# Kernel tuning notes

Hardware: AMD Instinct MI355X
Metric: run time of the kernel (lower is better)

The kernel has to match this reference:

```python
import jax, jax.numpy as jnp
import numpy as np

VOCAB, D, T, B, H, NCLS = 50000, 128, 512, 512, 100, 4


def setup_inputs() -> dict:
    key = jax.random.key(0)
    ks = jax.random.split(key, 7)
    tokens = jax.random.randint(ks[0], (B, T), 0, VOCAB, dtype=jnp.int32)
    emb = jax.random.normal(ks[1], (VOCAB, D), dtype=jnp.float32) * 0.05
    # Keras LSTM gate order: i, f, c(g), o packed along last dim (4H)
    kernel = jax.random.normal(ks[2], (D, 4 * H), dtype=jnp.float32) * (1.0 / np.sqrt(D))
    rec_kernel = jax.random.normal(ks[3], (H, 4 * H), dtype=jnp.float32) * (1.0 / np.sqrt(H))
    # unit_forget_bias: forget-gate bias initialized to 1
    bias = jnp.zeros((4 * H,), dtype=jnp.float32).at[H:2 * H].set(1.0)
    dense_w = jax.random.normal(ks[4], (H, NCLS), dtype=jnp.float32) * (1.0 / np.sqrt(H))
    dense_b = jnp.zeros((NCLS,), dtype=jnp.float32)
    return {"tokens": tokens, "emb": emb, "kernel": kernel,
            "rec_kernel": rec_kernel, "bias": bias,
            "dense_w": dense_w, "dense_b": dense_b}


def _lstm_last_hidden(x_tbd, kernel, rec_kernel, bias):
    # x_tbd: [T, B, D]. Precompute input projections for all steps (one big GEMM).
    xz = jnp.einsum('tbd,dg->tbg', x_tbd, kernel) + bias  # [T, B, 4H]

    def step(carry, xz_t):
        h, c = carry
        z = xz_t + h @ rec_kernel  # [B, 4H]
        i = jax.nn.sigmoid(z[:, 0 * H:1 * H])
        f = jax.nn.sigmoid(z[:, 1 * H:2 * H])
        g = jnp.tanh(z[:, 2 * H:3 * H])
        o = jax.nn.sigmoid(z[:, 3 * H:4 * H])
        c_new = f * c + i * g
        h_new = o * jnp.tanh(c_new)
        return (h_new, c_new), None

    bsz = x_tbd.shape[1]
    init = (jnp.zeros((bsz, H), x_tbd.dtype), jnp.zeros((bsz, H), x_tbd.dtype))
    (h_last, _), _ = jax.lax.scan(step, init, xz)
    return h_last  # [B, H]


def reference(tokens, emb, kernel, rec_kernel, bias, dense_w, dense_b):
    # Embedding lookup: [B, T] -> [B, T, D]
    x = emb[tokens]
    # SpatialDropout1D and LSTM dropout/recurrent_dropout are identity at inference.
    x_tbd = jnp.transpose(x, (1, 0, 2))  # [T, B, D]
    h = _lstm_last_hidden(x_tbd, kernel, rec_kernel, bias)  # [B, H]
    logits = h @ dense_w + dense_b  # [B, 4]
    return jax.nn.softmax(logits, axis=-1)
```

## Files before the change

kernel.cpp:

```cpp
#include <hip/hip_runtime.h>
#include <hip/hip_bf16.h>

#define VOCAB 50000
#define DD 128
#define TT 512
#define BB 512
#define HH 100
#define NCLS 4
#define NT 25
#define ROWS 4
#define NBLK (BB/ROWS)
#define NTHREADS 512
#define ZS 400

typedef short s16x8 __attribute__((ext_vector_type(8)));
typedef float f32x4 __attribute__((ext_vector_type(4)));

static __device__ __forceinline__ unsigned short f2b(float x) {
    __hip_bfloat16 h = __float2bfloat16(x);
    return __builtin_bit_cast(unsigned short, h);
}
static __device__ __forceinline__ float sigm(float x)  { return __fdividef(1.0f, 1.0f + __expf(-x)); }
static __device__ __forceinline__ float tanhx(float x) { return 1.0f - __fdividef(2.0f, 1.0f + __expf(2.0f * x)); }

#define BARRIER() asm volatile("s_waitcnt lgkmcnt(0)\n\ts_barrier" ::: "memory")

__global__ void cast_emb_k(const float* __restrict__ emb, unsigned short* __restrict__ out, int n4) {
    int i = blockIdx.x * blockDim.x + threadIdx.x;
    if (i < n4) {
        float4 v = reinterpret_cast<const float4*>(emb)[i];
        ushort4 o = make_ushort4(f2b(v.x), f2b(v.y), f2b(v.z), f2b(v.w));
        reinterpret_cast<ushort4*>(out)[i] = o;
    }
}

__global__ void build_frags_k(const float* __restrict__ kern, const float* __restrict__ rec,
                              unsigned short* __restrict__ ikf, unsigned short* __restrict__ recf) {
    int tid = blockIdx.x * blockDim.x + threadIdx.x;
    if (tid >= 2 * NT * 4 * 64) return;
    int tab  = tid / (NT * 4 * 64);
    int rem  = tid % (NT * 4 * 64);
    int lane = rem & 63;
    int fs   = rem >> 6;
    int ks   = fs & 3, nt = fs >> 2;
    int cp    = nt * 16 + (lane & 15);
    int oc    = (cp & 3) * 100 + (cp >> 2);
    int kbase = ks * 32 + (lane >> 4) * 8;
    unsigned short* dst = (tab ? recf : ikf) + rem * 8;
#pragma unroll
    for (int j = 0; j < 8; ++j) {
        int k = kbase + j;
        float v;
        if (tab == 0) v = kern[k * 400 + oc];
        else          v = (k < HH) ? rec[k * 400 + oc] : 0.0f;
        dst[j] = f2b(v);
    }
}

__global__ __launch_bounds__(NTHREADS, 2)
void lstm_fused2_k(const int* __restrict__ tokens,
                   const float* __restrict__ bias,
                   const float* __restrict__ dw,
                   const float* __restrict__ db,
                   const unsigned short* __restrict__ emb_bf,
                   const unsigned short* __restrict__ ikf_tab,
                   const unsigned short* __restrict__ recf_tab,
                   float* __restrict__ out)
{
    __shared__ __align__(16) unsigned short h_lds[2][16 * DD];
    __shared__ float z_lds[ROWS][ZS];
    __shared__ float hf_lds[ROWS * HH];
    __shared__ float dw_lds[HH * NCLS];
    __shared__ int   tok_lds[ROWS][TT];

    const int tid = threadIdx.x, lane = tid & 63, w = tid >> 6;
    const int lo = lane & 15, hi = lane >> 4;
    const int b0 = blockIdx.x * ROWS;
    const int nt0 = (w * NT) >> 3;
    const int cnt = (((w + 1) * NT) >> 3) - nt0;

    s16x8 ikf[4][4], rcf[4][4];
    float bv[4];
#pragma unroll
    for (int i = 0; i < 4; ++i) {
        if (i < cnt) {
            int cp = (nt0 + i) * 16 + lo;
            bv[i] = bias[(cp & 3) * 100 + (cp >> 2)];
#pragma unroll
            for (int ks = 0; ks < 4; ++ks) {
                ikf[i][ks] = *reinterpret_cast<const s16x8*>(ikf_tab  + (((nt0 + i) * 4 + ks) * 64 + lane) * 8);
                rcf[i][ks] = *reinterpret_cast<const s16x8*>(recf_tab + (((nt0 + i) * 4 + ks) * 64 + lane) * 8);
            }
        } else {
            bv[i] = 0.0f;
#pragma unroll
            for (int ks = 0; ks < 4; ++ks) { ikf[i][ks] = (s16x8)0; rcf[i][ks] = (s16x8)0; }
        }
    }
#pragma unroll
    for (int i = 0; i < 4; ++i) {
        asm volatile("" : "+v"(bv[i]));
#pragma unroll
        for (int ks = 0; ks < 4; ++ks) {
            asm volatile("" : "+v"(ikf[i][ks]));
            asm volatile("" : "+v"(rcf[i][ks]));
        }
    }

    for (int idx = tid; idx < 16 * DD; idx += NTHREADS)
        reinterpret_cast<unsigned int*>(&h_lds[0][0])[idx] = 0u;
    for (int idx = tid; idx < ROWS * TT; idx += NTHREADS)
        tok_lds[idx >> 9][idx & (TT - 1)] = tokens[(b0 + (idx >> 9)) * TT + (idx & (TT - 1))];
    if (tid < HH * NCLS) dw_lds[tid] = dw[tid];

    const int  grow = hi;
    const int  gjl  = lo;
    const bool g_on = gjl < 4 * cnt;
    float cst = 0.0f;

    const int xrow = lo & 3;
    int hof[4];
#pragma unroll
    for (int ks = 0; ks < 4; ++ks)
        hof[ks] = (lo * 256 + ks * 64 + hi * 16) ^ ((lo & 7) << 4);

    s16x8 xfA[4], xfB[4];
    {
        int t0 = tokens[(b0 + xrow) * TT + 0];
        int t1 = tokens[(b0 + xrow) * TT + 1];
#pragma unroll
        for (int ks = 0; ks < 4; ++ks) {
            xfA[ks] = *reinterpret_cast<const s16x8*>(emb_bf + (long)t0 * DD + ks * 32 + hi * 8);
            xfB[ks] = *reinterpret_cast<const s16x8*>(emb_bf + (long)t1 * DD + ks * 32 + hi * 8);
        }
    }
    __syncthreads();

    auto step = [&](int t, s16x8 (&xf)[4],
                    const unsigned short* hrd, unsigned short* hwr) {
        s16x8 hA[4];
#pragma unroll
        for (int ks = 0; ks < 4; ++ks)
            hA[ks] = *reinterpret_cast<const s16x8*>(reinterpret_cast<const char*>(hrd) + hof[ks]);

        f32x4 acc[4];
#pragma unroll
        for (int i = 0; i < 4; ++i) { acc[i][0] = bv[i]; acc[i][1] = bv[i]; acc[i][2] = bv[i]; acc[i][3] = bv[i]; }

#pragma unroll
        for (int ks = 0; ks < 4; ++ks)
#pragma unroll
            for (int i = 0; i < 4; ++i)
                if (i < cnt) acc[i] = __builtin_amdgcn_mfma_f32_16x16x32_bf16(xf[ks], ikf[i][ks], acc[i], 0, 0, 0);

        {
            int t2 = (t + 2 < TT) ? t + 2 : TT - 1;
            int tk = tok_lds[xrow][t2];
            const unsigned short* ep = emb_bf + (long)tk * DD;
#pragma unroll
            for (int ks = 0; ks < 4; ++ks)
                xf[ks] = *reinterpret_cast<const s16x8*>(ep + ks * 32 + hi * 8);
        }

#pragma unroll
        for (int ks = 0; ks < 4; ++ks)
#pragma unroll
            for (int i = 0; i < 4; ++i)
                if (i < cnt) acc[i] = __builtin_amdgcn_mfma_f32_16x16x32_bf16(hA[ks], rcf[i][ks], acc[i], 0, 0, 0);

        if (hi == 0) {
#pragma unroll
            for (int i = 0; i < 4; ++i) if (i < cnt)
#pragma unroll
                for (int r = 0; r < 4; ++r)
                    z_lds[r][(nt0 + i) * 16 + lo] = acc[i][r];
        }

        if (g_on) {
            float4 z4 = *reinterpret_cast<const float4*>(&z_lds[grow][nt0 * 16 + gjl * 4]);
            float ig = sigm(z4.x), fg = sigm(z4.y), gg = tanhx(z4.z), og = sigm(z4.w);
            cst = fg * cst + ig * gg;
            float hh = og * tanhx(cst);
            int j = nt0 * 4 + gjl;
            *reinterpret_cast<unsigned short*>(reinterpret_cast<char*>(hwr) +
                ((grow * 256 + j * 2) ^ (grow << 4))) = f2b(hh);
            if (t == TT - 1) hf_lds[grow * HH + j] = hh;
        }
        BARRIER();
    };

    for (int t = 0; t < TT; t += 2) {
        step(t,     xfA, h_lds[1], h_lds[0]);
        step(t + 1, xfB, h_lds[0], h_lds[1]);
    }

    if (tid < ROWS * NCLS) {
        int r = tid >> 2, c = tid & 3;
        float s = db[c];
#pragma unroll 4
        for (int k = 0; k < HH; ++k)
            s += hf_lds[r * HH + k] * dw_lds[k * NCLS + c];
        float mx = s;
        mx = fmaxf(mx, __shfl_xor(mx, 1));
        mx = fmaxf(mx, __shfl_xor(mx, 2));
        float e = __expf(s - mx);
        float den = e;
        den += __shfl_xor(den, 1);
        den += __shfl_xor(den, 2);
        out[(b0 + r) * NCLS + c] = e / den;
    }
}

extern "C" void kernel_launch(void* const* d_in, const int* in_sizes, int n_in,
                              void* d_out, int out_size, void* d_ws, size_t ws_size,
                              hipStream_t stream) {
    const int*   tokens = (const int*)d_in[0];
    const float* emb    = (const float*)d_in[1];
    const float* kern   = (const float*)d_in[2];
    const float* rec    = (const float*)d_in[3];
    const float* bias   = (const float*)d_in[4];
    const float* dw     = (const float*)d_in[5];
    const float* db     = (const float*)d_in[6];
    float* out = (float*)d_out;

    unsigned short* emb_bf = (unsigned short*)d_ws;
    unsigned short* ikf    = emb_bf + (size_t)VOCAB * DD;
    unsigned short* recf   = ikf + NT * 4 * 64 * 8;

    int n4 = VOCAB * DD / 4;
    cast_emb_k<<<(n4 + 255) / 256, 256, 0, stream>>>(emb, emb_bf, n4);
    build_frags_k<<<(2 * NT * 4 * 64 + 255) / 256, 256, 0, stream>>>(kern, rec, ikf, recf);
    lstm_fused2_k<<<NBLK, NTHREADS, 0, stream>>>(tokens, bias, dw, db, emb_bf, ikf, recf, out);
}
```

Baseline: 663.9 us.

## Swap MFMA operands so gates land in registers, removing z LDS round-trip

```diff
diff --git a/kernel.cpp b/kernel.cpp
--- a/kernel.cpp
+++ b/kernel.cpp
@@ -11,7 +11,6 @@
 #define ROWS 4
 #define NBLK (BB/ROWS)
 #define NTHREADS 512
-#define ZS 400
 
 typedef short s16x8 __attribute__((ext_vector_type(8)));
 typedef float f32x4 __attribute__((ext_vector_type(4)));
@@ -58,7 +57,7 @@
 }
 
 __global__ __launch_bounds__(NTHREADS, 2)
-void lstm_fused2_k(const int* __restrict__ tokens,
+void lstm_fused3_k(const int* __restrict__ tokens,
                    const float* __restrict__ bias,
                    const float* __restrict__ dw,
                    const float* __restrict__ db,
@@ -68,7 +67,6 @@
                    float* __restrict__ out)
 {
     __shared__ __align__(16) unsigned short h_lds[2][16 * DD];
-    __shared__ float z_lds[ROWS][ZS];
     __shared__ float hf_lds[ROWS * HH];
     __shared__ float dw_lds[HH * NCLS];
     __shared__ int   tok_lds[ROWS][TT];
@@ -80,26 +78,27 @@
     const int cnt = (((w + 1) * NT) >> 3) - nt0;
 
     s16x8 ikf[4][4], rcf[4][4];
-    float bv[4];
+    f32x4 bvq[4];
 #pragma unroll
     for (int i = 0; i < 4; ++i) {
         if (i < cnt) {
-            int cp = (nt0 + i) * 16 + lo;
-            bv[i] = bias[(cp & 3) * 100 + (cp >> 2)];
+#pragma unroll
+            for (int r = 0; r < 4; ++r)
+                bvq[i][r] = bias[r * 100 + (nt0 + i) * 4 + hi];
 #pragma unroll
             for (int ks = 0; ks < 4; ++ks) {
                 ikf[i][ks] = *reinterpret_cast<const s16x8*>(ikf_tab  + (((nt0 + i) * 4 + ks) * 64 + lane) * 8);
                 rcf[i][ks] = *reinterpret_cast<const s16x8*>(recf_tab + (((nt0 + i) * 4 + ks) * 64 + lane) * 8);
             }
         } else {
-            bv[i] = 0.0f;
+            bvq[i] = (f32x4)0.f;
 #pragma unroll
             for (int ks = 0; ks < 4; ++ks) { ikf[i][ks] = (s16x8)0; rcf[i][ks] = (s16x8)0; }
         }
     }
 #pragma unroll
     for (int i = 0; i < 4; ++i) {
-        asm volatile("" : "+v"(bv[i]));
+        asm volatile("" : "+v"(bvq[i]));
 #pragma unroll
         for (int ks = 0; ks < 4; ++ks) {
             asm volatile("" : "+v"(ikf[i][ks]));
@@ -113,12 +112,9 @@
         tok_lds[idx >> 9][idx & (TT - 1)] = tokens[(b0 + (idx >> 9)) * TT + (idx & (TT - 1))];
     if (tid < HH * NCLS) dw_lds[tid] = dw[tid];
 
-    const int  grow = hi;
-    const int  gjl  = lo;
-    const bool g_on = gjl < 4 * cnt;
-    float cst = 0.0f;
-
     const int xrow = lo & 3;
+    float cst[4] = {0.f, 0.f, 0.f, 0.f};
+
     int hof[4];
 #pragma unroll
     for (int ks = 0; ks < 4; ++ks)
@@ -138,20 +134,20 @@
 
     auto step = [&](int t, s16x8 (&xf)[4],
                     const unsigned short* hrd, unsigned short* hwr) {
-        s16x8 hA[4];
+        s16x8 hB[4];
 #pragma unroll
         for (int ks = 0; ks < 4; ++ks)
-            hA[ks] = *reinterpret_cast<const s16x8*>(reinterpret_cast<const char*>(hrd) + hof[ks]);
+            hB[ks] = *reinterpret_cast<const s16x8*>(reinterpret_cast<const char*>(hrd) + hof[ks]);
 
         f32x4 acc[4];
 #pragma unroll
-        for (int i = 0; i < 4; ++i) { acc[i][0] = bv[i]; acc[i][1] = bv[i]; acc[i][2] = bv[i]; acc[i][3] = bv[i]; }
+        for (int i = 0; i < 4; ++i) acc[i] = bvq[i];
 
 #pragma unroll
         for (int ks = 0; ks < 4; ++ks)
 #pragma unroll
             for (int i = 0; i < 4; ++i)
-                if (i < cnt) acc[i] = __builtin_amdgcn_mfma_f32_16x16x32_bf16(xf[ks], ikf[i][ks], acc[i], 0, 0, 0);
+                if (i < cnt) acc[i] = __builtin_amdgcn_mfma_f32_16x16x32_bf16(ikf[i][ks], xf[ks], acc[i], 0, 0, 0);
 
         {
             int t2 = (t + 2 < TT) ? t + 2 : TT - 1;
@@ -166,25 +162,25 @@
         for (int ks = 0; ks < 4; ++ks)
 #pragma unroll
             for (int i = 0; i < 4; ++i)
-                if (i < cnt) acc[i] = __builtin_amdgcn_mfma_f32_16x16x32_bf16(hA[ks], rcf[i][ks], acc[i], 0, 0, 0);
-
-        if (hi == 0) {
-#pragma unroll
-            for (int i = 0; i < 4; ++i) if (i < cnt)
-#pragma unroll
-                for (int r = 0; r < 4; ++r)
-                    z_lds[r][(nt0 + i) * 16 + lo] = acc[i][r];
-        }
-
-        if (g_on) {
-            float4 z4 = *reinterpret_cast<const float4*>(&z_lds[grow][nt0 * 16 + gjl * 4]);
-            float ig = sigm(z4.x), fg = sigm(z4.y), gg = tanhx(z4.z), og = sigm(z4.w);
-            cst = fg * cst + ig * gg;
-            float hh = og * tanhx(cst);
-            int j = nt0 * 4 + gjl;
-            *reinterpret_cast<unsigned short*>(reinterpret_cast<char*>(hwr) +
-                ((grow * 256 + j * 2) ^ (grow << 4))) = f2b(hh);
-            if (t == TT - 1) hf_lds[grow * HH + j] = hh;
+                if (i < cnt) acc[i] = __builtin_amdgcn_mfma_f32_16x16x32_bf16(rcf[i][ks], hB[ks], acc[i], 0, 0, 0);
+
+        if (lo < ROWS) {
+#pragma unroll
+            for (int i = 0; i < 4; ++i) if (i < cnt) {
+                float ig = sigm(acc[i][0]), fg = sigm(acc[i][1]);
+                float gg = tanhx(acc[i][2]), og = sigm(acc[i][3]);
+                cst[i] = fg * cst[i] + ig * gg;
+                float hh = og * tanhx(cst[i]);
+                unsigned short hb = f2b(hh);
+                int j2 = ((nt0 + i) * 4 + hi) * 2;
+#pragma unroll
+                for (int rep = 0; rep < 4; ++rep) {
+                    int row = lo + 4 * rep;
+                    *reinterpret_cast<unsigned short*>(reinterpret_cast<char*>(hwr) +
+                        ((row * 256 + j2) ^ ((row & 7) << 4))) = hb;
+                }
+                if (t == TT - 1) hf_lds[lo * HH + (j2 >> 1)] = hh;
+            }
         }
         BARRIER();
     };
@@ -230,5 +226,5 @@
     int n4 = VOCAB * DD / 4;
     cast_emb_k<<<(n4 + 255) / 256, 256, 0, stream>>>(emb, emb_bf, n4);
     build_frags_k<<<(2 * NT * 4 * 64 + 255) / 256, 256, 0, stream>>>(kern, rec, ikf, recf);
-    lstm_fused2_k<<<NBLK, NTHREADS, 0, stream>>>(tokens, bias, dw, db, emb_bf, ikf, recf, out);
-}
+    lstm_fused3_k<<<NBLK, NTHREADS, 0, stream>>>(tokens, bias, dw, db, emb_bf, ikf, recf, out);
+}
```

New measurement: 980.4 us. 1.48x slower.

## Software-pipeline input projection one step ahead and split recurrent MFMA chains

Applied to the files above, without the earlier changes.

```diff
diff --git a/kernel.cpp b/kernel.cpp
--- a/kernel.cpp
+++ b/kernel.cpp
@@ -22,6 +22,8 @@
 }
 static __device__ __forceinline__ float sigm(float x)  { return __fdividef(1.0f, 1.0f + __expf(-x)); }
 static __device__ __forceinline__ float tanhx(float x) { return 1.0f - __fdividef(2.0f, 1.0f + __expf(2.0f * x)); }
+
+#define MFMA(a, b, c) __builtin_amdgcn_mfma_f32_16x16x32_bf16((a), (b), (c), 0, 0, 0)
 
 #define BARRIER() asm volatile("s_waitcnt lgkmcnt(0)\n\ts_barrier" ::: "memory")
 
@@ -58,7 +60,7 @@
 }
 
 __global__ __launch_bounds__(NTHREADS, 2)
-void lstm_fused2_k(const int* __restrict__ tokens,
+void lstm_fused4_k(const int* __restrict__ tokens,
                    const float* __restrict__ bias,
                    const float* __restrict__ dw,
                    const float* __restrict__ db,
@@ -79,27 +81,30 @@
     const int nt0 = (w * NT) >> 3;
     const int cnt = (((w + 1) * NT) >> 3) - nt0;
 
+    const f32x4 zero4 = {0.f, 0.f, 0.f, 0.f};
+
     s16x8 ikf[4][4], rcf[4][4];
-    float bv[4];
+    f32x4 bq[4];
 #pragma unroll
     for (int i = 0; i < 4; ++i) {
         if (i < cnt) {
             int cp = (nt0 + i) * 16 + lo;
-            bv[i] = bias[(cp & 3) * 100 + (cp >> 2)];
+            float bs = bias[(cp & 3) * 100 + (cp >> 2)];
+            bq[i][0] = bs; bq[i][1] = bs; bq[i][2] = bs; bq[i][3] = bs;
 #pragma unroll
             for (int ks = 0; ks < 4; ++ks) {
                 ikf[i][ks] = *reinterpret_cast<const s16x8*>(ikf_tab  + (((nt0 + i) * 4 + ks) * 64 + lane) * 8);
                 rcf[i][ks] = *reinterpret_cast<const s16x8*>(recf_tab + (((nt0 + i) * 4 + ks) * 64 + lane) * 8);
             }
         } else {
-            bv[i] = 0.0f;
+            bq[i] = zero4;
 #pragma unroll
             for (int ks = 0; ks < 4; ++ks) { ikf[i][ks] = (s16x8)0; rcf[i][ks] = (s16x8)0; }
         }
     }
 #pragma unroll
     for (int i = 0; i < 4; ++i) {
-        asm volatile("" : "+v"(bv[i]));
+        asm volatile("" : "+v"(bq[i]));
 #pragma unroll
         for (int ks = 0; ks < 4; ++ks) {
             asm volatile("" : "+v"(ikf[i][ks]));
@@ -124,14 +129,30 @@
     for (int ks = 0; ks < 4; ++ks)
         hof[ks] = (lo * 256 + ks * 64 + hi * 16) ^ ((lo & 7) << 4);
 
+    f32x4 axa[4], axb[4];
     s16x8 xfA[4], xfB[4];
     {
-        int t0 = tokens[(b0 + xrow) * TT + 0];
-        int t1 = tokens[(b0 + xrow) * TT + 1];
+        int tk0 = tokens[(b0 + xrow) * TT + 0];
+        s16x8 x0[4];
+#pragma unroll
+        for (int ks = 0; ks < 4; ++ks)
+            x0[ks] = *reinterpret_cast<const s16x8*>(emb_bf + (long)tk0 * DD + ks * 32 + hi * 8);
+#pragma unroll
+        for (int i = 0; i < 4; ++i) {
+            axa[i] = MFMA(x0[0], ikf[i][0], zero4);
+            axb[i] = MFMA(x0[2], ikf[i][2], bq[i]);
+        }
+#pragma unroll
+        for (int i = 0; i < 4; ++i) {
+            axa[i] = MFMA(x0[1], ikf[i][1], axa[i]);
+            axb[i] = MFMA(x0[3], ikf[i][3], axb[i]);
+        }
+        int tk1 = tokens[(b0 + xrow) * TT + 1];
+        int tk2 = tokens[(b0 + xrow) * TT + 2];
 #pragma unroll
         for (int ks = 0; ks < 4; ++ks) {
-            xfA[ks] = *reinterpret_cast<const s16x8*>(emb_bf + (long)t0 * DD + ks * 32 + hi * 8);
-            xfB[ks] = *reinterpret_cast<const s16x8*>(emb_bf + (long)t1 * DD + ks * 32 + hi * 8);
+            xfA[ks] = *reinterpret_cast<const s16x8*>(emb_bf + (long)tk1 * DD + ks * 32 + hi * 8);
+            xfB[ks] = *reinterpret_cast<const s16x8*>(emb_bf + (long)tk2 * DD + ks * 32 + hi * 8);
         }
     }
     __syncthreads();
@@ -143,37 +164,44 @@
         for (int ks = 0; ks < 4; ++ks)
             hA[ks] = *reinterpret_cast<const s16x8*>(reinterpret_cast<const char*>(hrd) + hof[ks]);
 
-        f32x4 acc[4];
-#pragma unroll
-        for (int i = 0; i < 4; ++i) { acc[i][0] = bv[i]; acc[i][1] = bv[i]; acc[i][2] = bv[i]; acc[i][3] = bv[i]; }
-
-#pragma unroll
-        for (int ks = 0; ks < 4; ++ks)
-#pragma unroll
-            for (int i = 0; i < 4; ++i)
-                if (i < cnt) acc[i] = __builtin_amdgcn_mfma_f32_16x16x32_bf16(xf[ks], ikf[i][ks], acc[i], 0, 0, 0);
+        f32x4 ra[4], rb[4];
+#pragma unroll
+        for (int i = 0; i < 4; ++i) if (i < cnt) ra[i] = MFMA(hA[0], rcf[i][0], axa[i]);
+#pragma unroll
+        for (int i = 0; i < 4; ++i) if (i < cnt) rb[i] = MFMA(hA[2], rcf[i][2], axb[i]);
+
+#pragma unroll
+        for (int i = 0; i < 4; ++i) if (i < cnt) axa[i] = MFMA(xf[0], ikf[i][0], zero4);
+#pragma unroll
+        for (int i = 0; i < 4; ++i) if (i < cnt) axb[i] = MFMA(xf[2], ikf[i][2], bq[i]);
+
+#pragma unroll
+        for (int i = 0; i < 4; ++i) if (i < cnt) ra[i] = MFMA(hA[1], rcf[i][1], ra[i]);
+#pragma unroll
+        for (int i = 0; i < 4; ++i) if (i < cnt) rb[i] = MFMA(hA[3], rcf[i][3], rb[i]);
+
+#pragma unroll
+        for (int i = 0; i < 4; ++i) if (i < cnt) axa[i] = MFMA(xf[1], ikf[i][1], axa[i]);
+#pragma unroll
+        for (int i = 0; i < 4; ++i) if (i < cnt) axb[i] = MFMA(xf[3], ikf[i][3], axb[i]);
 
         {
-            int t2 = (t + 2 < TT) ? t + 2 : TT - 1;
-            int tk = tok_lds[xrow][t2];
+            int t3 = (t + 3 < TT) ? t + 3 : TT - 1;
+            int tk = tok_lds[xrow][t3];
             const unsigned short* ep = emb_bf + (long)tk * DD;
 #pragma unroll
             for (int ks = 0; ks < 4; ++ks)
                 xf[ks] = *reinterpret_cast<const s16x8*>(ep + ks * 32 + hi * 8);
         }
 
-#pragma unroll
-        for (int ks = 0; ks < 4; ++ks)
-#pragma unroll
-            for (int i = 0; i < 4; ++i)
-                if (i < cnt) acc[i] = __builtin_amdgcn_mfma_f32_16x16x32_bf16(hA[ks], rcf[i][ks], acc[i], 0, 0, 0);
-
         if (hi == 0) {
 #pragma unroll
-            for (int i = 0; i < 4; ++i) if (i < cnt)
+            for (int i = 0; i < 4; ++i) if (i < cnt) {
+                f32x4 zv = ra[i] + rb[i];
 #pragma unroll
                 for (int r = 0; r < 4; ++r)
-                    z_lds[r][(nt0 + i) * 16 + lo] = acc[i][r];
+                    z_lds[r][(nt0 + i) * 16 + lo] = zv[r];
+            }
         }
 
         if (g_on) {
@@ -230,5 +258,5 @@
     int n4 = VOCAB * DD / 4;
     cast_emb_k<<<(n4 + 255) / 256, 256, 0, stream>>>(emb, emb_bf, n4);
     build_frags_k<<<(2 * NT * 4 * 64 + 255) / 256, 256, 0, stream>>>(kern, rec, ikf, recf);
-    lstm_fused2_k<<<NBLK, NTHREADS, 0, stream>>>(tokens, bias, dw, db, emb_bf, ikf, recf, out);
-}
+    lstm_fused4_k<<<NBLK, NTHREADS, 0, stream>>>(tokens, bias, dw, db, emb_bf, ikf, recf, out);
+}
```

Result: slower. 965.1 us (+45.4%).
